# Kernel optimization log

Measured on AMD Instinct MI355X. Metric: run time of the kernel, lower is better.

The kernel has to match this reference:

```python
import jax, jax.numpy as jnp
import numpy as np

P, B, A, NT = 2, 96, 32, 24
N = B * A
MD, MA, MW = 4, 4, 2
NPOLB = MD + MA
C_LK = 0.089793561062583294  # 1 / (2 * pi**1.5)


def _norm(v):
    return v / jnp.sqrt(jnp.sum(v * v, -1, keepdims=True) + 1e-12)


def _gat_atoms(c, i):
    # c: [P,B,A,3], i: [P,B,K] -> [P,B,K,3]
    return jnp.take_along_axis(c, jnp.broadcast_to(i[..., None], i.shape + (3,)), axis=2)


def setup_inputs():
    key = jax.random.key(0)
    rng = np.random.default_rng(0)
    inp = {}
    inp["pose_coords"] = jax.random.normal(key, (P, N, 3), jnp.float32) * 8.0
    inp["pose_stack_block_type"] = jnp.asarray(rng.integers(0, NT, (P, B)), jnp.int32)
    inp["pose_stack_min_bond_separation"] = jnp.full((P, B, B), 6, jnp.int32)
    inp["bt_n_atoms"] = jnp.full((NT,), A, jnp.int32)
    bonds = np.stack([np.arange(A), (np.arange(A) + 1) % A], -1)
    inp["bt_all_bonds"] = jnp.asarray(np.broadcast_to(bonds, (NT, A, 2)).copy(), jnp.int32)
    rngs = np.stack([np.arange(A), np.arange(A) + 1], -1)
    inp["bt_atom_all_bond_ranges"] = jnp.asarray(np.broadcast_to(rngs, (NT, A, 2)).copy(), jnp.int32)
    inp["bt_tile_n_donH"] = jnp.asarray(rng.integers(1, MD + 1, (NT,)), jnp.int32)
    inp["bt_tile_n_acc"] = jnp.asarray(rng.integers(1, MA + 1, (NT,)), jnp.int32)
    donH = np.broadcast_to(2 * np.arange(MD) + 1, (NT, MD)).copy()
    inp["bt_tile_donH_inds"] = jnp.asarray(donH, jnp.int32)
    inp["bt_tile_don_hvy_inds"] = jnp.asarray(donH - 1, jnp.int32)
    inp["bt_tile_acc_inds"] = jnp.asarray(np.broadcast_to(8 + np.arange(MA), (NT, MA)).copy(), jnp.int32)
    inp["bt_tile_hybridization"] = jnp.asarray(rng.integers(0, 3, (NT, MA)), jnp.int32)
    is_h = np.zeros((NT, A), np.int32)
    is_h[:, 1:8:2] = 1
    inp["bt_atom_is_hydrogen"] = jnp.asarray(is_h)
    par = np.empty((NT, A, 4), np.float32)
    par[..., 0] = rng.uniform(1.4, 2.2, (NT, A))   # lj_radius
    par[..., 1] = rng.uniform(-6.0, 6.0, (NT, A))  # lk_dgfree
    par[..., 2] = rng.uniform(3.0, 3.6, (NT, A))   # lk_lambda
    par[..., 3] = rng.uniform(3.0, 15.0, (NT, A))  # lk_volume
    inp["bt_tile_lk_ball_params"] = jnp.asarray(par)
    pd = np.minimum(np.abs(np.arange(A)[:, None] - np.arange(A)[None, :]), 6)
    inp["bt_path_distance"] = jnp.asarray(np.broadcast_to(pd, (NT, A, A)).copy(), jnp.int32)
    inp["lk_ball_global_params"] = jnp.asarray([6.0, 3.709, 2.828], jnp.float32)   # cutoff, ramp_width_A2, d2_low
    inp["water_gen_global_params"] = jnp.asarray([2.65, 2.0943951], jnp.float32)   # water dist, water bond angle
    inp["sp2_water_tors"] = jnp.asarray([0.0, np.pi], jnp.float32)
    inp["sp3_water_tors"] = jnp.asarray([np.pi / 3.0, -np.pi / 3.0], jnp.float32)
    inp["ring_water_tors"] = jnp.asarray([0.0, np.pi / 2.0], jnp.float32)
    return inp


def reference(pose_coords, pose_stack_block_type, pose_stack_min_bond_separation,
              bt_n_atoms, bt_all_bonds, bt_atom_all_bond_ranges,
              bt_tile_n_donH, bt_tile_n_acc, bt_tile_donH_inds, bt_tile_don_hvy_inds,
              bt_tile_acc_inds, bt_tile_hybridization, bt_atom_is_hydrogen,
              bt_tile_lk_ball_params, bt_path_distance,
              lk_ball_global_params, water_gen_global_params,
              sp2_water_tors, sp3_water_tors, ring_water_tors):
    bt = pose_stack_block_type
    coords = pose_coords.reshape(P, B, A, 3)
    wdist = water_gen_global_params[0]
    wang = water_gen_global_params[1]
    # ---- step 1a: donor waters placed along heavy->H direction ----
    hvy_i = bt_tile_don_hvy_inds[bt]
    H_i = bt_tile_donH_inds[bt]                                              # [P,B,MD]
    hvy = _gat_atoms(coords, hvy_i)
    Hxyz = _gat_atoms(coords, H_i)
    don_w = hvy + wdist * _norm(Hxyz - hvy)                                  # [P,B,MD,3]
    don_mask = jnp.arange(MD) < bt_tile_n_donH[bt][..., None]                # [P,B,MD]
    don_w = jnp.broadcast_to(don_w[..., None, :], (P, B, MD, MW, 3))
    don_wm = don_mask[..., None] & (jnp.arange(MW) == 0)                     # one water per donH
    # ---- step 1b: acceptor waters via hybridization-dependent torsion (NeRF) ----
    acc_i = bt_tile_acc_inds[bt]                                             # [P,B,MA]
    ranges0 = bt_atom_all_bond_ranges[bt][..., 0]                            # [P,B,A]
    bonds1 = bt_all_bonds[bt][..., 1]                                        # [P,B,A]
    base_i = jnp.take_along_axis(bonds1, jnp.take_along_axis(ranges0, acc_i, axis=2), axis=2)
    base2_i = jnp.take_along_axis(bonds1, jnp.take_along_axis(ranges0, base_i, axis=2), axis=2)
    cxyz = _gat_atoms(coords, acc_i)
    bxyz = _gat_atoms(coords, base_i)
    axyz = _gat_atoms(coords, base2_i)
    e1 = _norm(cxyz - bxyz)
    nrm = _norm(jnp.cross(bxyz - axyz, e1))
    e2 = jnp.cross(nrm, e1)
    tors_tab = jnp.stack([sp2_water_tors, sp3_water_tors, ring_water_tors])  # [3,MW]
    chi = tors_tab[bt_tile_hybridization[bt]]                                # [P,B,MA,MW]
    ct, st = jnp.cos(wang), jnp.sin(wang)
    acc_w = (cxyz[..., None, :]
             + (-wdist * ct) * e1[..., None, :]
             + (wdist * st) * jnp.cos(chi)[..., None] * e2[..., None, :]
             + (wdist * st) * jnp.sin(chi)[..., None] * nrm[..., None, :])   # [P,B,MA,MW,3]
    acc_mask = jnp.arange(MA) < bt_tile_n_acc[bt][..., None]
    acc_wm = jnp.broadcast_to(acc_mask[..., None], (P, B, MA, MW))
    # ---- assemble polar sites + waters ----
    waters = jnp.concatenate([don_w, acc_w], axis=2).reshape(P, B * NPOLB, MW, 3)
    wmask = jnp.concatenate([don_wm, acc_wm], axis=2).reshape(P, B * NPOLB, MW)
    pol_loc = jnp.concatenate([hvy_i, acc_i], axis=2)                        # [P,B,NPOLB]
    pol_mask = jnp.concatenate([don_mask, acc_mask], axis=2).reshape(P, B * NPOLB)
    gidx = (jnp.arange(B)[None, :, None] * A + pol_loc).reshape(P, B * NPOLB)
    # ---- gather per-atom data ----
    params_flat = bt_tile_lk_ball_params[bt].reshape(P, N, 4)
    heavy = bt_atom_is_hydrogen[bt].reshape(P, N) == 0
    xp = jnp.take_along_axis(pose_coords, jnp.broadcast_to(gidx[..., None], gidx.shape + (3,)), axis=1)
    pp = jnp.take_along_axis(params_flat, jnp.broadcast_to(gidx[..., None], gidx.shape + (4,)), axis=1)
    # ---- step 2: pair distances + bond-separation mask ----
    diff = xp[:, :, None, :] - pose_coords[:, None, :, :]                    # [P,NPOL,N,3]
    d2 = jnp.maximum(jnp.sum(diff * diff, -1), 1e-2)
    d = jnp.sqrt(d2)
    b_i = gidx // A
    a_i = gidx % A
    b_j = jnp.arange(N) // A
    a_j = jnp.arange(N) % A
    bti = jnp.take_along_axis(bt, b_i, axis=1)
    intra = bt_path_distance[bti[:, :, None], a_i[:, :, None], a_j[None, None, :]]
    inter = pose_stack_min_bond_separation[jnp.arange(P)[:, None, None], b_i[:, :, None], b_j[None, None, :]]
    sep = jnp.where(b_i[:, :, None] == b_j[None, None, :], intra, inter)
    cutoff = lk_ball_global_params[0]
    ramp2 = lk_ball_global_params[1]
    d2_low = lk_ball_global_params[2]
    mask = (sep >= 4) & heavy[:, None, :] & pol_mask[:, :, None] & (d < cutoff)
    # ---- isotropic LK desolvation of polar atom i by occluder j ----
    ri, dgi, lami = pp[..., 0], pp[..., 1], pp[..., 2]
    rj, volj = params_flat[..., 0], params_flat[..., 3]
    x = (d - (ri[:, :, None] + rj[:, None, :])) / lami[:, :, None]
    lk_iso = C_LK * dgi[:, :, None] * volj[:, None, :] / lami[:, :, None] * jnp.exp(-x * x) / d2
    lk_iso = jnp.where(mask, lk_iso, 0.0)
    # ---- lk-ball fraction from water-site occlusion ----
    wdiff = waters[:, :, :, None, :] - pose_coords[:, None, None, :, :]      # [P,NPOL,MW,N,3]
    d2w = jnp.sum(wdiff * wdiff, -1)
    d2w = jnp.where(wmask[..., None], d2w, 1e9)
    d2wmin = jnp.min(d2w, axis=2)                                            # [P,NPOL,N]
    wt = jnp.clip((d2_low + ramp2 - d2wmin) / ramp2, 0.0, 1.0)
    frac = wt * wt * (3.0 - 2.0 * wt)
    return jnp.stack([jnp.sum(lk_iso, (1, 2)), jnp.sum(lk_iso * frac, (1, 2))])  # [2,P]
```

## Files before the change

### kernel.cpp

```cpp
#include <hip/hip_runtime.h>
#include <math.h>

constexpr int P  = 2;
constexpr int B  = 96;
constexpr int A  = 32;
constexpr int N  = B * A;
constexpr int MD = 4;
constexpr int MA = 4;
constexpr int NPOL = MD + MA;
constexpr int SJ = 2;
constexpr int JS = N / SJ;
constexpr int JPT = JS / 256;
constexpr int NB = P * B * SJ;
constexpr float C_LK  = 0.0897935610625833f;
constexpr float LOG2E = 1.4426950408889634f;


__global__ __launch_bounds__(256) void lkball_kernel(
    const float* __restrict__ pose_coords,
    const int*   __restrict__ block_type,
    const int*   __restrict__ min_sep,
    const int*   __restrict__ all_bonds,
    const int*   __restrict__ bond_ranges,
    const int*   __restrict__ n_donH,
    const int*   __restrict__ n_acc,
    const int*   __restrict__ donH_inds,
    const int*   __restrict__ don_hvy_inds,
    const int*   __restrict__ acc_inds,
    const int*   __restrict__ hyb,
    const int*   __restrict__ is_h,
    const float* __restrict__ lk_params,
    const int*   __restrict__ path_dist,
    const float* __restrict__ glob,
    const float* __restrict__ wglob,
    const float* __restrict__ sp2t,
    const float* __restrict__ sp3t,
    const float* __restrict__ ringt,
    float*       __restrict__ ws)
{
    __shared__ float spolar[NPOL][16];
    __shared__ int   spolai[NPOL];
    __shared__ int   s_bt[B];
    __shared__ int   smsep[B];
    __shared__ int   spath[NPOL * A];
    __shared__ float red0[4], red1[4];

    const int bid   = blockIdx.x;
    const int p     = bid / (B * SJ);
    const int rem   = bid % (B * SJ);
    const int b     = rem / SJ;
    const int slice = rem % SJ;
    const int tid   = threadIdx.x;

    if (tid < NPOL) {
        const int k  = tid;
        const int bt = block_type[p * B + b];
        const float wdist = wglob[0];
        const float wang  = wglob[1];
        float xp[3], w0[3], w1[3];
        int   a_i, valid;
        if (k < MD) {
            valid = (k < n_donH[bt]) ? 1 : 0;
            const int hvy = don_hvy_inds[bt * MD + k];
            const int Hi  = donH_inds[bt * MD + k];
            a_i = hvy;
            const float* hc = pose_coords + (size_t)(p * N + b * A + hvy) * 3;
            const float* Hc = pose_coords + (size_t)(p * N + b * A + Hi) * 3;
            float dx = Hc[0] - hc[0], dy = Hc[1] - hc[1], dz = Hc[2] - hc[2];
            float inv = 1.0f / sqrtf(dx * dx + dy * dy + dz * dz + 1e-12f);
            xp[0] = hc[0]; xp[1] = hc[1]; xp[2] = hc[2];
            w0[0] = hc[0] + wdist * dx * inv;
            w0[1] = hc[1] + wdist * dy * inv;
            w0[2] = hc[2] + wdist * dz * inv;
            w1[0] = hc[0] + 1.0e3f; w1[1] = hc[1] + 1.0e3f; w1[2] = hc[2] + 1.0e3f;
        } else {
            const int kk = k - MD;
            valid = (kk < n_acc[bt]) ? 1 : 0;
            const int ai = acc_inds[bt * MA + kk];
            a_i = ai;
            const int r0    = bond_ranges[(bt * A + ai) * 2 + 0];
            const int base  = all_bonds[(bt * A + r0) * 2 + 1];
            const int r0b   = bond_ranges[(bt * A + base) * 2 + 0];
            const int base2 = all_bonds[(bt * A + r0b) * 2 + 1];
            const float* c  = pose_coords + (size_t)(p * N + b * A + ai)    * 3;
            const float* bx = pose_coords + (size_t)(p * N + b * A + base)  * 3;
            const float* ax = pose_coords + (size_t)(p * N + b * A + base2) * 3;

            float e1x = c[0] - bx[0], e1y = c[1] - bx[1], e1z = c[2] - bx[2];
            float inv1 = 1.0f / sqrtf(e1x * e1x + e1y * e1y + e1z * e1z + 1e-12f);
            e1x *= inv1; e1y *= inv1; e1z *= inv1;

            float ux = bx[0] - ax[0], uy = bx[1] - ax[1], uz = bx[2] - ax[2];
            float nx = uy * e1z - uz * e1y;
            float ny = uz * e1x - ux * e1z;
            float nz = ux * e1y - uy * e1x;
            float inv2 = 1.0f / sqrtf(nx * nx + ny * ny + nz * nz + 1e-12f);
            nx *= inv2; ny *= inv2; nz *= inv2;
            float e2x = ny * e1z - nz * e1y;
            float e2y = nz * e1x - nx * e1z;
            float e2z = nx * e1y - ny * e1x;

            const int hy = hyb[bt * MA + kk];
            const float* tab = (hy == 0) ? sp2t : ((hy == 1) ? sp3t : ringt);
            const float ct = cosf(wang), st = sinf(wang);
            float c0 = cosf(tab[0]), s0 = sinf(tab[0]);
            float c1 = cosf(tab[1]), s1 = sinf(tab[1]);

            xp[0] = c[0]; xp[1] = c[1]; xp[2] = c[2];
            w0[0] = c[0] - wdist * ct * e1x + wdist * st * c0 * e2x + wdist * st * s0 * nx;
            w0[1] = c[1] - wdist * ct * e1y + wdist * st * c0 * e2y + wdist * st * s0 * ny;
            w0[2] = c[2] - wdist * ct * e1z + wdist * st * c0 * e2z + wdist * st * s0 * nz;
            w1[0] = c[0] - wdist * ct * e1x + wdist * st * c1 * e2x + wdist * st * s1 * nx;
            w1[1] = c[1] - wdist * ct * e1y + wdist * st * c1 * e2y + wdist * st * s1 * ny;
            w1[2] = c[2] - wdist * ct * e1z + wdist * st * c1 * e2z + wdist * st * s1 * nz;
        }
        const float* pr = lk_params + (size_t)(bt * A + a_i) * 4;
        const float lam = pr[2];
        spolar[k][0] = xp[0]; spolar[k][1] = xp[1]; spolar[k][2] = xp[2];
        spolar[k][3] = w0[0]; spolar[k][4] = w0[1]; spolar[k][5] = w0[2];
        spolar[k][6] = w1[0]; spolar[k][7] = w1[1]; spolar[k][8] = w1[2];
        spolar[k][9]  = pr[0];
        spolar[k][10] = valid ? (C_LK * pr[1] / lam) : 0.0f;
        spolar[k][11] = -LOG2E / (lam * lam);
        spolai[k] = a_i;
    }
    if (tid >= 64 && tid < 64 + B)   s_bt[tid - 64]   = block_type[p * B + (tid - 64)];
    if (tid >= 160 && tid < 160 + B) smsep[tid - 160] = min_sep[(p * B + b) * B + (tid - 160)];
    __syncthreads();

    {
        const int k  = tid >> 5;
        const int aj = tid & 31;
        const int bt = s_bt[b];
        spath[tid] = path_dist[(bt * A + spolai[k]) * A + aj];
    }
    __syncthreads();

    const float cutoff2   = glob[0] * glob[0];
    const float inv_ramp2 = 1.0f / glob[1];
    const float c4        = (glob[2] + glob[1]) * inv_ramp2;
    const int a_j   = tid & 31;
    const int jbase = slice * JS + tid;

    float cx[JPT], cy[JPT], cz[JPT], rj[JPT], ve[JPT], msep_f[JPT];
    int   intra[JPT];
#pragma unroll
    for (int i = 0; i < JPT; ++i) {
        const int j   = jbase + 256 * i;
        const int b_j = j >> 5;
        const float* cj = pose_coords + (size_t)(p * N + j) * 3;
        cx[i] = cj[0]; cy[i] = cj[1]; cz[i] = cj[2];
        const int bt_j = s_bt[b_j];
        const int hv   = is_h[bt_j * A + a_j];
        const float4 pj = *(const float4*)(lk_params + (size_t)(bt_j * A + a_j) * 4);
        rj[i] = pj.x;
        ve[i] = hv ? 0.0f : pj.w;
        msep_f[i] = (float)smsep[b_j];
        intra[i]  = (b_j == b);
    }

    float acc0 = 0.0f, acc1 = 0.0f;

#pragma unroll
    for (int k = 0; k < MD; ++k) {
        const float4 q0 = ((const float4*)spolar[k])[0];
        const float4 q1 = ((const float4*)spolar[k])[1];
        const float4 q2 = ((const float4*)spolar[k])[2];
        const float px  = q0.x, py  = q0.y, pz  = q0.z;
        const float w0x = q0.w, w0y = q1.x, w0z = q1.y;
        const float ri  = q2.y, pref = q2.z, negq = q2.w;
        const float path_k = (float)spath[k * A + a_j];

#pragma unroll
        for (int i = 0; i < JPT; ++i) {
            const float dx = px - cx[i], dy = py - cy[i], dz = pz - cz[i];
            float d2 = fmaf(dx, dx, fmaf(dy, dy, dz * dz));
            d2 = fmaxf(d2, 0.01f);
            const float rinv = __builtin_amdgcn_rsqf(d2);
            const float d = d2 * rinv;
            const float sep = intra[i] ? path_k : msep_f[i];
            const bool ok = (sep >= 4.0f) & (d2 < cutoff2);

            const float t = d - ri - rj[i];
            const float e = __builtin_amdgcn_exp2f(t * t * negq);
            float lk = pref * ve[i] * e * (rinv * rinv);
            lk = ok ? lk : 0.0f;

            const float d0x = w0x - cx[i], d0y = w0y - cy[i], d0z = w0z - cz[i];
            const float d2wmin = fmaf(d0x, d0x, fmaf(d0y, d0y, d0z * d0z));
            float wt = fmaf(d2wmin, -inv_ramp2, c4);
            wt = fminf(fmaxf(wt, 0.0f), 1.0f);
            const float frac = wt * wt * fmaf(-2.0f, wt, 3.0f);

            acc0 += lk;
            acc1 = fmaf(lk, frac, acc1);
        }
    }

#pragma unroll
    for (int k = MD; k < NPOL; ++k) {
        const float4 q0 = ((const float4*)spolar[k])[0];
        const float4 q1 = ((const float4*)spolar[k])[1];
        const float4 q2 = ((const float4*)spolar[k])[2];
        const float px  = q0.x, py  = q0.y, pz  = q0.z;
        const float w0x = q0.w, w0y = q1.x, w0z = q1.y;
        const float w1x = q1.z, w1y = q1.w, w1z = q2.x;
        const float ri  = q2.y, pref = q2.z, negq = q2.w;
        const float path_k = (float)spath[k * A + a_j];

#pragma unroll
        for (int i = 0; i < JPT; ++i) {
            const float dx = px - cx[i], dy = py - cy[i], dz = pz - cz[i];
            float d2 = fmaf(dx, dx, fmaf(dy, dy, dz * dz));
            d2 = fmaxf(d2, 0.01f);
            const float rinv = __builtin_amdgcn_rsqf(d2);
            const float d = d2 * rinv;
            const float sep = intra[i] ? path_k : msep_f[i];
            const bool ok = (sep >= 4.0f) & (d2 < cutoff2);

            const float t = d - ri - rj[i];
            const float e = __builtin_amdgcn_exp2f(t * t * negq);
            float lk = pref * ve[i] * e * (rinv * rinv);
            lk = ok ? lk : 0.0f;

            const float d0x = w0x - cx[i], d0y = w0y - cy[i], d0z = w0z - cz[i];
            const float d1x = w1x - cx[i], d1y = w1y - cy[i], d1z = w1z - cz[i];
            const float d2w0 = fmaf(d0x, d0x, fmaf(d0y, d0y, d0z * d0z));
            const float d2w1 = fmaf(d1x, d1x, fmaf(d1y, d1y, d1z * d1z));
            const float d2wmin = fminf(d2w0, d2w1);
            float wt = fmaf(d2wmin, -inv_ramp2, c4);
            wt = fminf(fmaxf(wt, 0.0f), 1.0f);
            const float frac = wt * wt * fmaf(-2.0f, wt, 3.0f);

            acc0 += lk;
            acc1 = fmaf(lk, frac, acc1);
        }
    }

    for (int off = 32; off > 0; off >>= 1) {
        acc0 += __shfl_down(acc0, off);
        acc1 += __shfl_down(acc1, off);
    }
    const int wave = tid >> 6;
    const int lane = tid & 63;
    if (lane == 0) { red0[wave] = acc0; red1[wave] = acc1; }
    __syncthreads();
    if (tid == 0) {
        ws[bid]       = red0[0] + red0[1] + red0[2] + red0[3];
        ws[512 + bid] = red1[0] + red1[1] + red1[2] + red1[3];
    }
}

__global__ __launch_bounds__(256) void reduce_kernel(
    const float* __restrict__ ws, float* __restrict__ out)
{
    const int wave = threadIdx.x >> 6;
    const int lane = threadIdx.x & 63;
    const int base = (wave & 1) * (B * SJ) + (wave >> 1) * 512;
    float s = 0.0f;
    for (int i = lane; i < B * SJ; i += 64) s += ws[base + i];
    for (int off = 32; off > 0; off >>= 1) s += __shfl_down(s, off);
    if (lane == 0) out[(wave >> 1) * P + (wave & 1)] = s;
}

extern "C" void kernel_launch(void* const* d_in, const int* in_sizes, int n_in,
                              void* d_out, int out_size, void* d_ws, size_t ws_size,
                              hipStream_t stream) {
    const float* pose_coords  = (const float*)d_in[0];
    const int*   block_type   = (const int*)  d_in[1];
    const int*   min_sep      = (const int*)  d_in[2];
    const int*   all_bonds    = (const int*)  d_in[4];
    const int*   bond_ranges  = (const int*)  d_in[5];
    const int*   n_donH       = (const int*)  d_in[6];
    const int*   n_acc        = (const int*)  d_in[7];
    const int*   donH_inds    = (const int*)  d_in[8];
    const int*   don_hvy_inds = (const int*)  d_in[9];
    const int*   acc_inds     = (const int*)  d_in[10];
    const int*   hyb          = (const int*)  d_in[11];
    const int*   is_h         = (const int*)  d_in[12];
    const float* lk_params    = (const float*)d_in[13];
    const int*   path_dist    = (const int*)  d_in[14];
    const float* glob         = (const float*)d_in[15];
    const float* wglob        = (const float*)d_in[16];
    const float* sp2t         = (const float*)d_in[17];
    const float* sp3t         = (const float*)d_in[18];
    const float* ringt        = (const float*)d_in[19];
    float* out = (float*)d_out;
    float* ws  = (float*)d_ws;

    lkball_kernel<<<NB, 256, 0, stream>>>(
        pose_coords, block_type, min_sep, all_bonds, bond_ranges,
        n_donH, n_acc, donH_inds, don_hvy_inds, acc_inds, hyb, is_h,
        lk_params, path_dist, glob, wglob, sp2t, sp3t, ringt, ws);

    reduce_kernel<<<1, 256, 0, stream>>>(ws, out);
}
```

Before: 106.7 us.

## Split occluder range into four slices and drop a barrier in setup

Doubles the number of j-slices per residue block, going from 384 to 768 workgroups with half as many occluder atoms per thread, so the 256 CUs on MI355X get more parallel work. The path-distance table is now loaded directly from global indices instead of through a shared-memory index array, which removes one __syncthreads. Per-polar-atom sums (ri+rj, pref*ve) are hoisted out of the inner loop. In exchange, each block repeats the polar-site setup more often, and the workspace offsets are widened to fit the larger block count.

```diff
diff --git a/kernel.cpp b/kernel.cpp
--- a/kernel.cpp
+++ b/kernel.cpp
@@ -8,10 +8,11 @@
 constexpr int MD = 4;
 constexpr int MA = 4;
 constexpr int NPOL = MD + MA;
-constexpr int SJ = 2;
+constexpr int SJ = 4;
 constexpr int JS = N / SJ;
 constexpr int JPT = JS / 256;
 constexpr int NB = P * B * SJ;
+constexpr int PB = B * SJ;
 constexpr float C_LK  = 0.0897935610625833f;
 constexpr float LOG2E = 1.4426950408889634f;
 
@@ -39,30 +40,37 @@
     float*       __restrict__ ws)
 {
     __shared__ float spolar[NPOL][16];
-    __shared__ int   spolai[NPOL];
     __shared__ int   s_bt[B];
     __shared__ int   smsep[B];
     __shared__ int   spath[NPOL * A];
     __shared__ float red0[4], red1[4];
 
     const int bid   = blockIdx.x;
-    const int p     = bid / (B * SJ);
-    const int rem   = bid % (B * SJ);
+    const int p     = bid / PB;
+    const int rem   = bid % PB;
     const int b     = rem / SJ;
     const int slice = rem % SJ;
     const int tid   = threadIdx.x;
 
+    const int bt_b = block_type[p * B + b];
+
+    {
+        const int k  = tid >> 5;
+        const int aj = tid & 31;
+        const int ak = (k < MD) ? don_hvy_inds[bt_b * MD + k]
+                                : acc_inds[bt_b * MA + (k - MD)];
+        spath[tid] = path_dist[(bt_b * A + ak) * A + aj];
+    }
     if (tid < NPOL) {
         const int k  = tid;
-        const int bt = block_type[p * B + b];
         const float wdist = wglob[0];
         const float wang  = wglob[1];
         float xp[3], w0[3], w1[3];
         int   a_i, valid;
         if (k < MD) {
-            valid = (k < n_donH[bt]) ? 1 : 0;
-            const int hvy = don_hvy_inds[bt * MD + k];
-            const int Hi  = donH_inds[bt * MD + k];
+            valid = (k < n_donH[bt_b]) ? 1 : 0;
+            const int hvy = don_hvy_inds[bt_b * MD + k];
+            const int Hi  = donH_inds[bt_b * MD + k];
             a_i = hvy;
             const float* hc = pose_coords + (size_t)(p * N + b * A + hvy) * 3;
             const float* Hc = pose_coords + (size_t)(p * N + b * A + Hi) * 3;
@@ -75,13 +83,13 @@
             w1[0] = hc[0] + 1.0e3f; w1[1] = hc[1] + 1.0e3f; w1[2] = hc[2] + 1.0e3f;
         } else {
             const int kk = k - MD;
-            valid = (kk < n_acc[bt]) ? 1 : 0;
-            const int ai = acc_inds[bt * MA + kk];
+            valid = (kk < n_acc[bt_b]) ? 1 : 0;
+            const int ai = acc_inds[bt_b * MA + kk];
             a_i = ai;
-            const int r0    = bond_ranges[(bt * A + ai) * 2 + 0];
-            const int base  = all_bonds[(bt * A + r0) * 2 + 1];
-            const int r0b   = bond_ranges[(bt * A + base) * 2 + 0];
-            const int base2 = all_bonds[(bt * A + r0b) * 2 + 1];
+            const int r0    = bond_ranges[(bt_b * A + ai) * 2 + 0];
+            const int base  = all_bonds[(bt_b * A + r0) * 2 + 1];
+            const int r0b   = bond_ranges[(bt_b * A + base) * 2 + 0];
+            const int base2 = all_bonds[(bt_b * A + r0b) * 2 + 1];
             const float* c  = pose_coords + (size_t)(p * N + b * A + ai)    * 3;
             const float* bx = pose_coords + (size_t)(p * N + b * A + base)  * 3;
             const float* ax = pose_coords + (size_t)(p * N + b * A + base2) * 3;
@@ -100,7 +108,7 @@
             float e2y = nz * e1x - nx * e1z;
             float e2z = nx * e1y - ny * e1x;
 
-            const int hy = hyb[bt * MA + kk];
+            const int hy = hyb[bt_b * MA + kk];
             const float* tab = (hy == 0) ? sp2t : ((hy == 1) ? sp3t : ringt);
             const float ct = cosf(wang), st = sinf(wang);
             float c0 = cosf(tab[0]), s0 = sinf(tab[0]);
@@ -114,7 +122,7 @@
             w1[1] = c[1] - wdist * ct * e1y + wdist * st * c1 * e2y + wdist * st * s1 * ny;
             w1[2] = c[2] - wdist * ct * e1z + wdist * st * c1 * e2z + wdist * st * s1 * nz;
         }
-        const float* pr = lk_params + (size_t)(bt * A + a_i) * 4;
+        const float* pr = lk_params + (size_t)(bt_b * A + a_i) * 4;
         const float lam = pr[2];
         spolar[k][0] = xp[0]; spolar[k][1] = xp[1]; spolar[k][2] = xp[2];
         spolar[k][3] = w0[0]; spolar[k][4] = w0[1]; spolar[k][5] = w0[2];
@@ -122,18 +130,9 @@
         spolar[k][9]  = pr[0];
         spolar[k][10] = valid ? (C_LK * pr[1] / lam) : 0.0f;
         spolar[k][11] = -LOG2E / (lam * lam);
-        spolai[k] = a_i;
     }
     if (tid >= 64 && tid < 64 + B)   s_bt[tid - 64]   = block_type[p * B + (tid - 64)];
     if (tid >= 160 && tid < 160 + B) smsep[tid - 160] = min_sep[(p * B + b) * B + (tid - 160)];
-    __syncthreads();
-
-    {
-        const int k  = tid >> 5;
-        const int aj = tid & 31;
-        const int bt = s_bt[b];
-        spath[tid] = path_dist[(bt * A + spolai[k]) * A + aj];
-    }
     __syncthreads();
 
     const float cutoff2   = glob[0] * glob[0];
@@ -171,6 +170,10 @@
         const float ri  = q2.y, pref = q2.z, negq = q2.w;
         const float path_k = (float)spath[k * A + a_j];
 
+        float rij[JPT], pv[JPT];
+#pragma unroll
+        for (int i = 0; i < JPT; ++i) { rij[i] = ri + rj[i]; pv[i] = pref * ve[i]; }
+
 #pragma unroll
         for (int i = 0; i < JPT; ++i) {
             const float dx = px - cx[i], dy = py - cy[i], dz = pz - cz[i];
@@ -181,9 +184,9 @@
             const float sep = intra[i] ? path_k : msep_f[i];
             const bool ok = (sep >= 4.0f) & (d2 < cutoff2);
 
-            const float t = d - ri - rj[i];
+            const float t = d - rij[i];
             const float e = __builtin_amdgcn_exp2f(t * t * negq);
-            float lk = pref * ve[i] * e * (rinv * rinv);
+            float lk = pv[i] * e * (rinv * rinv);
             lk = ok ? lk : 0.0f;
 
             const float d0x = w0x - cx[i], d0y = w0y - cy[i], d0z = w0z - cz[i];
@@ -208,6 +211,10 @@
         const float ri  = q2.y, pref = q2.z, negq = q2.w;
         const float path_k = (float)spath[k * A + a_j];
 
+        float rij[JPT], pv[JPT];
+#pragma unroll
+        for (int i = 0; i < JPT; ++i) { rij[i] = ri + rj[i]; pv[i] = pref * ve[i]; }
+
 #pragma unroll
         for (int i = 0; i < JPT; ++i) {
             const float dx = px - cx[i], dy = py - cy[i], dz = pz - cz[i];
@@ -218,9 +225,9 @@
             const float sep = intra[i] ? path_k : msep_f[i];
             const bool ok = (sep >= 4.0f) & (d2 < cutoff2);
 
-            const float t = d - ri - rj[i];
+            const float t = d - rij[i];
             const float e = __builtin_amdgcn_exp2f(t * t * negq);
-            float lk = pref * ve[i] * e * (rinv * rinv);
+            float lk = pv[i] * e * (rinv * rinv);
             lk = ok ? lk : 0.0f;
 
             const float d0x = w0x - cx[i], d0y = w0y - cy[i], d0z = w0z - cz[i];
@@ -246,8 +253,8 @@
     if (lane == 0) { red0[wave] = acc0; red1[wave] = acc1; }
     __syncthreads();
     if (tid == 0) {
-        ws[bid]       = red0[0] + red0[1] + red0[2] + red0[3];
-        ws[512 + bid] = red1[0] + red1[1] + red1[2] + red1[3];
+        ws[bid]        = red0[0] + red0[1] + red0[2] + red0[3];
+        ws[1024 + bid] = red1[0] + red1[1] + red1[2] + red1[3];
     }
 }
 
@@ -256,9 +263,9 @@
 {
     const int wave = threadIdx.x >> 6;
     const int lane = threadIdx.x & 63;
-    const int base = (wave & 1) * (B * SJ) + (wave >> 1) * 512;
+    const int base = (wave >> 1) * 1024 + (wave & 1) * PB;
     float s = 0.0f;
-    for (int i = lane; i < B * SJ; i += 64) s += ws[base + i];
+    for (int i = lane; i < PB; i += 64) s += ws[base + i];
     for (int off = 32; off > 0; off >>= 1) s += __shfl_down(s, off);
     if (lane == 0) out[(wave >> 1) * P + (wave & 1)] = s;
 }
```

Measured after the change: 104.3 us. 1.02x faster.
